# Performance work log

Hardware: AMD Instinct MI355X
Metric: run time of the kernel (lower is better)

## Reference

```python
import jax, jax.numpy as jnp
import numpy as np

PAD = -999
BATCH, NCHAIN, SEQ, NALT, NRES = 8, 2, 1024, 3, 20
NATOMS = 2_000_000
NATNAMES = 40
BACKBONE = jnp.array([0, 1, 2, 3], dtype=jnp.int32)  # N, CA, C, O atom-name ids
GLY = 7  # residue id treated as glycine (rsaSC forced to 0)
NBINS = BATCH * NCHAIN * SEQ * NALT


def setup_inputs() -> dict:
    key = jax.random.key(0)
    k = jax.random.split(key, 8)
    contRat = jax.random.uniform(k[0], (NATOMS, NALT), dtype=jnp.float32)
    atname = jax.random.randint(k[1], (NATOMS,), 0, NATNAMES, dtype=jnp.int32)
    # assign each atom to a (batch, chain, resnum) residue consistently
    resid = jax.random.randint(k[2], (NATOMS,), 0, BATCH * NCHAIN * SEQ, dtype=jnp.int32)
    batch = resid // (NCHAIN * SEQ)
    chain = (resid // SEQ) % NCHAIN
    resnum = resid % SEQ
    # residue type is a function of the residue (consistent across its atoms)
    resname_per_res = jax.random.randint(k[3], (BATCH * NCHAIN * SEQ,), 0, NRES, dtype=jnp.int32)
    resname = resname_per_res[resid]
    atom_description = jnp.stack([atname, resnum, chain, batch, resname], axis=1)
    alternatives = jax.random.bernoulli(k[4], 0.7, (NATOMS, NALT))
    # per-residue-type affine normalization points (max, min), max > min
    resMC_min = jax.random.uniform(k[5], (NRES,), dtype=jnp.float32) * 2.0
    resMC_max = resMC_min + 10.0 + jax.random.uniform(k[6], (NRES,), dtype=jnp.float32) * 20.0
    resSC_min = jax.random.uniform(k[7], (NRES,), dtype=jnp.float32) * 2.0
    resSC_max = resSC_min + 10.0 + jax.random.uniform(jax.random.fold_in(key, 99), (NRES,), dtype=jnp.float32) * 20.0
    return {
        "contRat": contRat,
        "resMC_max": resMC_max,
        "resMC_min": resMC_min,
        "resSC_max": resSC_max,
        "resSC_min": resSC_min,
        "atom_description": atom_description,
        "alternatives": alternatives,
    }


def _bind(contRat, resMC_max, resMC_min, resSC_max, resSC_min, atom_description, alternatives):
    atname = atom_description[:, 0]
    resnum = atom_description[:, 1]
    chain = atom_description[:, 2]
    batchInd = atom_description[:, 3]
    resname = atom_description[:, 4]

    is_backbone = jnp.isin(atname, BACKBONE)
    valid = atname != PAD

    # flat (batch, chain, resnum, alt) bin per atom per alternative
    base = (batchInd * NCHAIN + chain) * SEQ + resnum            # [natoms]
    flat = base[:, None] * NALT + jnp.arange(NALT, dtype=jnp.int32)[None, :]  # [natoms, nalt]

    maskMC = alternatives & (is_backbone & valid)[:, None]
    maskSC = alternatives & (~is_backbone & valid)[:, None]

    zero_idx = jnp.where(maskMC, flat, 0)
    rsaMC = jnp.zeros((NBINS,), contRat.dtype).at[zero_idx].add(
        jnp.where(maskMC, contRat, 0.0))
    rsaSC = jnp.zeros((NBINS,), contRat.dtype).at[jnp.where(maskSC, flat, 0)].add(
        jnp.where(maskSC, contRat, 0.0))

    # sequence: non-accumulating scatter of resname on the backbone path; dump
    # masked-out writes to an extra trailing bin
    seq_flat = jnp.full((NBINS + 1,), PAD, dtype=jnp.int32).at[
        jnp.where(maskMC, flat, NBINS)
    ].set(jnp.where(maskMC, resname[:, None], PAD))[:NBINS]

    shape = (BATCH, NCHAIN, SEQ, NALT)
    rsaMC = rsaMC.reshape(shape)
    rsaSC = rsaSC.reshape(shape)
    seq = seq_flat.reshape(shape)

    # per-residue-type affine normalization: (x - min) / (max - min)
    idx = jnp.clip(seq, 0, NRES - 1)
    has_res = seq != PAD
    rsaMC = jnp.where(has_res, (rsaMC - resMC_min[idx]) / (resMC_max[idx] - resMC_min[idx]), rsaMC)
    sc_norm = (rsaSC - resSC_min[idx]) / (resSC_max[idx] - resSC_min[idx])
    rsaSC = jnp.where(has_res & (seq != GLY), sc_norm,
                      jnp.where(has_res & (seq == GLY), 0.0, rsaSC))

    return jnp.clip(rsaMC, 0.0, 1.0), jnp.clip(rsaSC, 0.0, 1.0)


def reference(contRat, resMC_max, resMC_min, resSC_max, resSC_min, atom_description, alternatives):
    return _bind(contRat, resMC_max, resMC_min, resSC_max, resSC_min,
                 atom_description, alternatives)
```

## Files before the change

kernel.cpp:

```cpp
#include <hip/hip_runtime.h>


#define PADV   (-999)
#define BATCH  8
#define NCHAIN 2
#define SEQL   1024
#define NALT   3
#define NRES   20
#define NATOMS 2000000
#define GLY    7
#define NRESID (BATCH * NCHAIN * SEQL)
#define NBINS  (NRESID * NALT)
#define NBLK   ((NATOMS + 1023) / 1024)
#define NBUCK  256
#define ACC_SUB 8

#define PK_R(w)    ((int)((w) & 16383u))
#define PK_RES(w)  (((w) >> 14) & 31u)
#define PK_BB(w)   (((w) >> 19) & 1u)
#define PK_AM(w)   ((w) >> 20)

#define OFF_PACK  ((size_t)0)
#define SZ_PACK   ((size_t)NATOMS * 4)
#define OFF_HIST  (OFF_PACK + SZ_PACK)
#define SZ_HIST   ((size_t)NBUCK * NBLK * 4)
#define OFF_BB    (OFF_HIST + SZ_HIST)
#define SZ_BB     ((size_t)1280)
#define OFF_TOT   (OFF_BB + SZ_BB)
#define SZ_TOT    ((size_t)1024)
#define OFF_SORT  (OFF_TOT + SZ_TOT)
#define SZ_SORT   ((size_t)NATOMS * 8)
#define OFF_ACC   (OFF_SORT + SZ_SORT)
#define SZ_ACC    ((size_t)NBUCK * ACC_SUB * 384 * 4)
#define OFF_RES   (OFF_ACC + SZ_ACC)
#define SZ_RES    ((size_t)NBUCK * ACC_SUB * 64 * 4)
#define WS_NEED   (OFF_RES + SZ_RES)

__global__ __launch_bounds__(256)
void k_pack_hist(const int* __restrict__ desc,
                 const unsigned char* __restrict__ altB,
                 const int* __restrict__ altI,
                 unsigned* __restrict__ pack,
                 unsigned* __restrict__ hist) {
    __shared__ unsigned h[NBUCK];
    for (int j = threadIdx.x; j < NBUCK; j += 256) h[j] = 0u;
    __syncthreads();

    const unsigned char probe = altB[(threadIdx.x & 63) * 4 + 1];
    const bool byteLayout = (__ballot(probe != 0) != 0ULL);

    const int a0 = (blockIdx.x * 256 + threadIdx.x) * 4;
    if (a0 < NATOMS) {
        const int4* d4 = (const int4*)(desc + (size_t)a0 * 5);
        int4 q0 = d4[0], q1 = d4[1], q2 = d4[2], q3 = d4[3], q4 = d4[4];
        int an[4], rn[4], ch[4], bi[4], rs[4];
        an[0]=q0.x; rn[0]=q0.y; ch[0]=q0.z; bi[0]=q0.w; rs[0]=q1.x;
        an[1]=q1.y; rn[1]=q1.z; ch[1]=q1.w; bi[1]=q2.x; rs[1]=q2.y;
        an[2]=q2.z; rn[2]=q2.w; ch[2]=q3.x; bi[2]=q3.y; rs[2]=q3.z;
        an[3]=q3.w; rn[3]=q4.x; ch[3]=q4.y; bi[3]=q4.z; rs[3]=q4.w;

        unsigned am[4];
        if (byteLayout) {
            const unsigned* b3 = (const unsigned*)(altB + (size_t)a0 * 3);
            unsigned w0 = b3[0], w1 = b3[1], w2 = b3[2];
            unsigned char f[12];
            f[0]=w0; f[1]=w0>>8; f[2]=w0>>16; f[3]=w0>>24;
            f[4]=w1; f[5]=w1>>8; f[6]=w1>>16; f[7]=w1>>24;
            f[8]=w2; f[9]=w2>>8; f[10]=w2>>16; f[11]=w2>>24;
            #pragma unroll
            for (int k = 0; k < 4; ++k)
                am[k] = (f[k*3+0]?1u:0u) | (f[k*3+1]?2u:0u) | (f[k*3+2]?4u:0u);
        } else {
            const int4* i4 = (const int4*)(altI + (size_t)a0 * 3);
            int4 w0 = i4[0], w1 = i4[1], w2 = i4[2];
            int f[12] = {w0.x,w0.y,w0.z,w0.w, w1.x,w1.y,w1.z,w1.w,
                         w2.x,w2.y,w2.z,w2.w};
            #pragma unroll
            for (int k = 0; k < 4; ++k)
                am[k] = (f[k*3+0]?1u:0u) | (f[k*3+1]?2u:0u) | (f[k*3+2]?4u:0u);
        }

        uint4 pw;
        unsigned* pwp = (unsigned*)&pw;
        #pragma unroll
        for (int k = 0; k < 4; ++k) {
            const bool valid = (an[k] != PADV);
            const bool bb    = ((unsigned)an[k] <= 3u);
            const int  r     = (bi[k] * NCHAIN + ch[k]) * SEQL + rn[k];
            const bool rOK   = ((unsigned)r < (unsigned)NRESID);
            const unsigned a = (valid && rOK) ? am[k] : 0u;
            pwp[k] = (rOK ? (unsigned)r : 0u)
                   | ((unsigned)(rs[k] & 31) << 14)
                   | ((bb ? 1u : 0u) << 19) | (a << 20);
            if (a) atomicAdd(&h[(pwp[k] >> 6) & 255u], 1u);
        }
        *(uint4*)(pack + a0) = pw;
    }
    __syncthreads();
    for (int j = threadIdx.x; j < NBUCK; j += 256)
        hist[(size_t)j * NBLK + blockIdx.x] = h[j];
}

__global__ __launch_bounds__(256)
void k_prefix1(unsigned* __restrict__ hist, unsigned* __restrict__ totals) {
    __shared__ unsigned cnt[2048];
    __shared__ unsigned csum[256];
    unsigned* h = hist + (size_t)blockIdx.x * NBLK;
    const int t = threadIdx.x;

    for (int j = t; j < 2048; j += 256) cnt[j] = (j < NBLK) ? h[j] : 0u;
    __syncthreads();

    unsigned s = 0;
    #pragma unroll
    for (int k = 0; k < 8; ++k) s += cnt[t * 8 + k];
    csum[t] = s;
    __syncthreads();
    for (int off = 1; off < 256; off <<= 1) {
        unsigned x = (t >= off) ? csum[t - off] : 0u;
        __syncthreads();
        csum[t] += x;
        __syncthreads();
    }
    if (t == 255) totals[blockIdx.x] = csum[255];
    unsigned run = (t == 0) ? 0u : csum[t - 1];
    #pragma unroll
    for (int k = 0; k < 8; ++k) {
        const int idx = t * 8 + k;
        const unsigned old = cnt[idx];
        cnt[idx] = run;
        run += old;
    }
    __syncthreads();
    for (int j = t; j < NBLK; j += 256) h[j] = cnt[j];
}

__global__ __launch_bounds__(256)
void k_prefix2(const unsigned* __restrict__ totals,
               unsigned* __restrict__ bucketBase) {
    __shared__ unsigned s[256];
    const int t = threadIdx.x;
    const unsigned own = totals[t];
    s[t] = own;
    __syncthreads();
    for (int off = 1; off < 256; off <<= 1) {
        unsigned x = (t >= off) ? s[t - off] : 0u;
        __syncthreads();
        s[t] += x;
        __syncthreads();
    }
    bucketBase[t] = s[t] - own;
    if (t == 255) bucketBase[256] = s[255];
}

__global__ __launch_bounds__(256)
void k_scatter(const unsigned* __restrict__ pack,
               const unsigned* __restrict__ hist,
               const unsigned* __restrict__ bucketBase,
               uint2* __restrict__ sorted) {
    __shared__ unsigned lbase[NBUCK];
    for (int j = threadIdx.x; j < NBUCK; j += 256)
        lbase[j] = bucketBase[j] + hist[(size_t)j * NBLK + blockIdx.x];
    __syncthreads();

    const int a0 = (blockIdx.x * 256 + threadIdx.x) * 4;
    if (a0 < NATOMS) {
        const uint4 pw = *(const uint4*)(pack + a0);
        const unsigned* pwp = (const unsigned*)&pw;
        #pragma unroll
        for (int k = 0; k < 4; ++k) {
            const unsigned w = pwp[k];
            if (w >> 20) {
                const unsigned b   = (w >> 6) & 255u;
                const unsigned pos = atomicAdd(&lbase[b], 1u);
                sorted[pos] = make_uint2(w, (unsigned)(a0 + k));
            }
        }
    }
}

__global__ __launch_bounds__(256)
void k_accum(const uint2* __restrict__ sorted,
             const float* __restrict__ contRat,
             const unsigned* __restrict__ bucketBase,
             float* __restrict__ accPart,
             unsigned* __restrict__ resPart) {
    __shared__ float acc[6 * 64];
    __shared__ unsigned ror[64];
    const int b   = blockIdx.x >> 3;
    const int sub = blockIdx.x & 7;

    for (int j = threadIdx.x; j < 384; j += 256) acc[j] = 0.0f;
    if (threadIdx.x < 64) ror[threadIdx.x] = 0u;
    __syncthreads();

    const unsigned s0 = bucketBase[b], s1 = bucketBase[b + 1];
    const unsigned len = s1 - s0;
    const unsigned lo = s0 + (unsigned)(((unsigned long long)len * sub) >> 3);
    const unsigned hi = s0 + (unsigned)(((unsigned long long)len * (sub + 1)) >> 3);

    for (unsigned i = lo + threadIdx.x; i < hi; i += 256) {
        const uint2 e = sorted[i];
        const unsigned w = e.x;
        const int lr = (int)(w & 63u);
        const unsigned am = PK_AM(w);
        const float* cr = contRat + (size_t)e.y * 3;
        const int pb = PK_BB(w) ? 0 : 3;
        if (PK_BB(w)) atomicOr(&ror[lr], (am << 5) | PK_RES(w));
        if (am & 1) atomicAdd(&acc[(pb + 0) * 64 + lr], cr[0]);
        if (am & 2) atomicAdd(&acc[(pb + 1) * 64 + lr], cr[1]);
        if (am & 4) atomicAdd(&acc[(pb + 2) * 64 + lr], cr[2]);
    }
    __syncthreads();

    float* ap = accPart + ((size_t)b * ACC_SUB + sub) * 384;
    for (int j = threadIdx.x; j < 384; j += 256) ap[j] = acc[j];
    if (threadIdx.x < 64)
        resPart[((size_t)b * ACC_SUB + sub) * 64 + threadIdx.x] = ror[threadIdx.x];
}

__global__ __launch_bounds__(192)
void k_finalize(const float* __restrict__ accPart,
                const unsigned* __restrict__ resPart,
                float* __restrict__ out,
                const float* __restrict__ mcmax,
                const float* __restrict__ mcmin,
                const float* __restrict__ scmax,
                const float* __restrict__ scmin) {
    const int b = blockIdx.x;
    const int t = threadIdx.x;
    const int lr = t / 3, alt = t - lr * 3;

    float m = 0.0f, v = 0.0f;
    unsigned rb = 0u;
    #pragma unroll
    for (int s = 0; s < ACC_SUB; ++s) {
        const float* ap = accPart + ((size_t)b * ACC_SUB + s) * 384;
        m  += ap[alt * 64 + lr];
        v  += ap[(3 + alt) * 64 + lr];
        rb |= resPart[((size_t)b * ACC_SUB + s) * 64 + lr];
    }

    if ((rb >> (5 + alt)) & 1u) {
        int resn = (int)(rb & 31u);
        if (resn > NRES - 1) resn = NRES - 1;
        m = (m - mcmin[resn]) / (mcmax[resn] - mcmin[resn]);
        v = ((rb & 31u) == GLY) ? 0.0f
                                : (v - scmin[resn]) / (scmax[resn] - scmin[resn]);
    }
    out[b * 192 + t]         = fminf(fmaxf(m, 0.0f), 1.0f);
    out[NBINS + b * 192 + t] = fminf(fmaxf(v, 0.0f), 1.0f);
}

__global__ void k_init_flat(float* __restrict__ out, int* __restrict__ seq,
                            int* __restrict__ flag,
                            const unsigned char* __restrict__ altBytes) {
    int i = blockIdx.x * blockDim.x + threadIdx.x;
    if (i < NBINS) { out[i] = 0.0f; out[NBINS + i] = 0.0f; seq[i] = PADV; }
    if (blockIdx.x == 0 && threadIdx.x < 64) {
        unsigned char b = altBytes[threadIdx.x * 4 + 1];
        unsigned long long m = __ballot(b != 0);
        if (threadIdx.x == 0) *flag = (m != 0ULL) ? 1 : 0;
    }
}

__global__ void k_scatter_flat(const float* __restrict__ contRat,
                               const int* __restrict__ desc,
                               const unsigned char* __restrict__ altB,
                               const int* __restrict__ altI,
                               const int* __restrict__ flag,
                               float* __restrict__ mcArr,
                               float* __restrict__ scArr,
                               int* __restrict__ seq) {
    int a = blockIdx.x * blockDim.x + threadIdx.x;
    if (a >= NATOMS) return;
    const int atname  = desc[a * 5 + 0];
    const int resnum  = desc[a * 5 + 1];
    const int chain   = desc[a * 5 + 2];
    const int batchI  = desc[a * 5 + 3];
    const int resname = desc[a * 5 + 4];
    const bool valid = (atname != PADV);
    const bool is_bb = (atname >= 0) && (atname <= 3);
    const int  base  = ((batchI * NCHAIN + chain) * SEQL + resnum) * NALT;
    const bool byteLayout = (*flag != 0);
    #pragma unroll
    for (int alt = 0; alt < NALT; ++alt) {
        bool altv;
        if (byteLayout) altv = (altB[a * NALT + alt] != 0);
        else            altv = (altI[a * NALT + alt] != 0);
        if (altv && valid) {
            const float c = contRat[a * NALT + alt];
            const int   f = base + alt;
            if (is_bb) { atomicAdd(&mcArr[f], c); seq[f] = resname; }
            else       { atomicAdd(&scArr[f], c); }
        }
    }
}

__global__ void k_final_flat(float* __restrict__ mc, float* __restrict__ sc,
                             const int* __restrict__ seq,
                             const float* __restrict__ mcmax,
                             const float* __restrict__ mcmin,
                             const float* __restrict__ scmax,
                             const float* __restrict__ scmin) {
    int i = blockIdx.x * blockDim.x + threadIdx.x;
    if (i >= NBINS) return;
    const int s = seq[i];
    float m = mc[i], v = sc[i];
    if (s != PADV) {
        int idx = s < 0 ? 0 : (s > NRES - 1 ? NRES - 1 : s);
        m = (m - mcmin[idx]) / (mcmax[idx] - mcmin[idx]);
        if (s != GLY) v = (v - scmin[idx]) / (scmax[idx] - scmin[idx]);
        else          v = 0.0f;
    }
    mc[i] = fminf(fmaxf(m, 0.0f), 1.0f);
    sc[i] = fminf(fmaxf(v, 0.0f), 1.0f);
}

extern "C" void kernel_launch(void* const* d_in, const int* in_sizes, int n_in,
                              void* d_out, int out_size, void* d_ws, size_t ws_size,
                              hipStream_t stream) {
    const float* contRat = (const float*)d_in[0];
    const float* mcmax   = (const float*)d_in[1];
    const float* mcmin   = (const float*)d_in[2];
    const float* scmax   = (const float*)d_in[3];
    const float* scmin   = (const float*)d_in[4];
    const int*   desc    = (const int*)d_in[5];
    const void*  alts    = d_in[6];

    float* out = (float*)d_out;

    if (ws_size >= WS_NEED) {
        unsigned* pack  = (unsigned*)((char*)d_ws + OFF_PACK);
        unsigned* hist  = (unsigned*)((char*)d_ws + OFF_HIST);
        unsigned* bbase = (unsigned*)((char*)d_ws + OFF_BB);
        unsigned* tot   = (unsigned*)((char*)d_ws + OFF_TOT);
        uint2*    sorted= (uint2*)   ((char*)d_ws + OFF_SORT);
        float*    accP  = (float*)   ((char*)d_ws + OFF_ACC);
        unsigned* resP  = (unsigned*)((char*)d_ws + OFF_RES);

        k_pack_hist<<<NBLK, 256, 0, stream>>>(
            desc, (const unsigned char*)alts, (const int*)alts, pack, hist);
        k_prefix1<<<NBUCK, 256, 0, stream>>>(hist, tot);
        k_prefix2<<<1, 256, 0, stream>>>(tot, bbase);
        k_scatter<<<NBLK, 256, 0, stream>>>(pack, hist, bbase, sorted);
        k_accum<<<NBUCK * ACC_SUB, 256, 0, stream>>>(
            sorted, contRat, bbase, accP, resP);
        k_finalize<<<NBUCK, 192, 0, stream>>>(
            accP, resP, out, mcmax, mcmin, scmax, scmin);
    } else {
        int* seq  = (int*)d_ws;
        int* flag = seq + NBINS;
        const int binBlocks = (NBINS + 255) / 256;
        k_init_flat<<<binBlocks, 256, 0, stream>>>(out, seq, flag,
                                                   (const unsigned char*)alts);
        k_scatter_flat<<<(NATOMS + 255) / 256, 256, 0, stream>>>(
            contRat, desc,
            (const unsigned char*)alts, (const int*)alts, flag,
            out, out + NBINS, seq);
        k_final_flat<<<binBlocks, 256, 0, stream>>>(
            out, out + NBINS, seq, mcmax, mcmin, scmax, scmin);
    }
}
```

Baseline: 170.1 us.

## Fuse prefix/finalize kernels, coalesce scatter via shared-memory local sort, enlarge atom blocks

Each block now handles 4096 atoms, which cuts the histogram to 489 columns and lets prefix1 scan it with two values per thread. The separate bucket-base scan kernel is removed and its scan is recomputed inside scatter and accum. Scatter first sorts its atoms locally in shared memory, then writes to the global sorted array in bucket-contiguous runs instead of uncoalesced atomic-slot writes. Finalize is merged into accum: the last of the 8 sub-blocks per bucket, chosen by a ticket counter, does the reduction. This saves two launches, at the cost of repeated 256-wide scans per block and about 40KB of extra shared memory in scatter.

```diff
diff --git a/kernel.cpp b/kernel.cpp
--- a/kernel.cpp
+++ b/kernel.cpp
@@ -11,7 +11,8 @@
 #define GLY    7
 #define NRESID (BATCH * NCHAIN * SEQL)
 #define NBINS  (NRESID * NALT)
-#define NBLK   ((NATOMS + 1023) / 1024)
+#define APB    4096
+#define NBLK   ((NATOMS + APB - 1) / APB)
 #define NBUCK  256
 #define ACC_SUB 8
 
@@ -24,11 +25,11 @@
 #define SZ_PACK   ((size_t)NATOMS * 4)
 #define OFF_HIST  (OFF_PACK + SZ_PACK)
 #define SZ_HIST   ((size_t)NBUCK * NBLK * 4)
-#define OFF_BB    (OFF_HIST + SZ_HIST)
-#define SZ_BB     ((size_t)1280)
-#define OFF_TOT   (OFF_BB + SZ_BB)
+#define OFF_TOT   (OFF_HIST + SZ_HIST)
 #define SZ_TOT    ((size_t)1024)
-#define OFF_SORT  (OFF_TOT + SZ_TOT)
+#define OFF_TKT   (OFF_TOT + SZ_TOT)
+#define SZ_TKT    ((size_t)1024)
+#define OFF_SORT  (OFF_TKT + SZ_TKT)
 #define SZ_SORT   ((size_t)NATOMS * 8)
 #define OFF_ACC   (OFF_SORT + SZ_SORT)
 #define SZ_ACC    ((size_t)NBUCK * ACC_SUB * 384 * 4)
@@ -43,14 +44,18 @@
                  unsigned* __restrict__ pack,
                  unsigned* __restrict__ hist) {
     __shared__ unsigned h[NBUCK];
-    for (int j = threadIdx.x; j < NBUCK; j += 256) h[j] = 0u;
+    h[threadIdx.x] = 0u;
     __syncthreads();
 
     const unsigned char probe = altB[(threadIdx.x & 63) * 4 + 1];
     const bool byteLayout = (__ballot(probe != 0) != 0ULL);
 
-    const int a0 = (blockIdx.x * 256 + threadIdx.x) * 4;
-    if (a0 < NATOMS) {
+    const int blockBase = blockIdx.x * APB;
+    #pragma unroll
+    for (int g = 0; g < 4; ++g) {
+        const int a0 = blockBase + (g * 256 + (int)threadIdx.x) * 4;
+        if (a0 >= NATOMS) continue;
+
         const int4* d4 = (const int4*)(desc + (size_t)a0 * 5);
         int4 q0 = d4[0], q1 = d4[1], q2 = d4[2], q3 = d4[3], q4 = d4[4];
         int an[4], rn[4], ch[4], bi[4], rs[4];
@@ -97,23 +102,23 @@
         *(uint4*)(pack + a0) = pw;
     }
     __syncthreads();
-    for (int j = threadIdx.x; j < NBUCK; j += 256)
-        hist[(size_t)j * NBLK + blockIdx.x] = h[j];
+    hist[(size_t)threadIdx.x * NBLK + blockIdx.x] = h[threadIdx.x];
 }
 
 __global__ __launch_bounds__(256)
-void k_prefix1(unsigned* __restrict__ hist, unsigned* __restrict__ totals) {
-    __shared__ unsigned cnt[2048];
+void k_prefix1(unsigned* __restrict__ hist,
+               unsigned* __restrict__ totals,
+               unsigned* __restrict__ ticket) {
+    __shared__ unsigned cnt[512];
     __shared__ unsigned csum[256];
     unsigned* h = hist + (size_t)blockIdx.x * NBLK;
     const int t = threadIdx.x;
 
-    for (int j = t; j < 2048; j += 256) cnt[j] = (j < NBLK) ? h[j] : 0u;
-    __syncthreads();
-
-    unsigned s = 0;
-    #pragma unroll
-    for (int k = 0; k < 8; ++k) s += cnt[t * 8 + k];
+    cnt[t]       = (t < NBLK) ? h[t] : 0u;
+    cnt[t + 256] = (t + 256 < NBLK) ? h[t + 256] : 0u;
+    __syncthreads();
+
+    unsigned s = cnt[2 * t] + cnt[2 * t + 1];
     csum[t] = s;
     __syncthreads();
     for (int off = 1; off < 256; off <<= 1) {
@@ -122,84 +127,145 @@
         csum[t] += x;
         __syncthreads();
     }
-    if (t == 255) totals[blockIdx.x] = csum[255];
+    if (t == 0) { totals[blockIdx.x] = csum[255]; ticket[blockIdx.x] = 0u; }
+
     unsigned run = (t == 0) ? 0u : csum[t - 1];
-    #pragma unroll
-    for (int k = 0; k < 8; ++k) {
-        const int idx = t * 8 + k;
-        const unsigned old = cnt[idx];
-        cnt[idx] = run;
-        run += old;
-    }
-    __syncthreads();
-    for (int j = t; j < NBLK; j += 256) h[j] = cnt[j];
-}
-
-__global__ __launch_bounds__(256)
-void k_prefix2(const unsigned* __restrict__ totals,
-               unsigned* __restrict__ bucketBase) {
-    __shared__ unsigned s[256];
-    const int t = threadIdx.x;
-    const unsigned own = totals[t];
-    s[t] = own;
-    __syncthreads();
-    for (int off = 1; off < 256; off <<= 1) {
-        unsigned x = (t >= off) ? s[t - off] : 0u;
-        __syncthreads();
-        s[t] += x;
-        __syncthreads();
-    }
-    bucketBase[t] = s[t] - own;
-    if (t == 255) bucketBase[256] = s[255];
+    const unsigned c0 = cnt[2 * t];
+    cnt[2 * t]     = run;
+    cnt[2 * t + 1] = run + c0;
+    __syncthreads();
+    if (t < NBLK)       h[t]       = cnt[t];
+    if (t + 256 < NBLK) h[t + 256] = cnt[t + 256];
 }
 
 __global__ __launch_bounds__(256)
 void k_scatter(const unsigned* __restrict__ pack,
                const unsigned* __restrict__ hist,
-               const unsigned* __restrict__ bucketBase,
+               const unsigned* __restrict__ totals,
                uint2* __restrict__ sorted) {
-    __shared__ unsigned lbase[NBUCK];
-    for (int j = threadIdx.x; j < NBUCK; j += 256)
-        lbase[j] = bucketBase[j] + hist[(size_t)j * NBLK + blockIdx.x];
-    __syncthreads();
-
-    const int a0 = (blockIdx.x * 256 + threadIdx.x) * 4;
-    if (a0 < NATOMS) {
-        const uint4 pw = *(const uint4*)(pack + a0);
-        const unsigned* pwp = (const unsigned*)&pw;
+    __shared__ unsigned sc[256];
+    __shared__ unsigned gBase[256];
+    __shared__ unsigned lofs[256];
+    __shared__ unsigned lcnt[256];
+    __shared__ unsigned wBuf[APB];
+    __shared__ unsigned idxBuf[APB];
+
+    const int t   = threadIdx.x;
+    const int blk = blockIdx.x;
+
+    const unsigned own = totals[t];
+    sc[t] = own;
+    __syncthreads();
+    for (int off = 1; off < 256; off <<= 1) {
+        unsigned x = (t >= off) ? sc[t - off] : 0u;
+        __syncthreads();
+        sc[t] += x;
+        __syncthreads();
+    }
+    gBase[t] = (sc[t] - own) + hist[(size_t)t * NBLK + blk];
+    lcnt[t] = 0u;
+    __syncthreads();
+
+    const int blockBase = blk * APB;
+    uint4 pw[4];
+    #pragma unroll
+    for (int g = 0; g < 4; ++g) {
+        const int a0 = blockBase + (g * 256 + t) * 4;
+        if (a0 < NATOMS) {
+            pw[g] = *(const uint4*)(pack + a0);
+            const unsigned* p = (const unsigned*)&pw[g];
+            #pragma unroll
+            for (int k = 0; k < 4; ++k)
+                if (p[k] >> 20) atomicAdd(&lcnt[(p[k] >> 6) & 255u], 1u);
+        } else {
+            pw[g] = make_uint4(0u, 0u, 0u, 0u);
+        }
+    }
+    __syncthreads();
+
+    const unsigned lown = lcnt[t];
+    sc[t] = lown;
+    __syncthreads();
+    for (int off = 1; off < 256; off <<= 1) {
+        unsigned x = (t >= off) ? sc[t - off] : 0u;
+        __syncthreads();
+        sc[t] += x;
+        __syncthreads();
+    }
+    lofs[t] = sc[t] - lown;
+    lcnt[t] = 0u;
+    __syncthreads();
+    const unsigned total = sc[255];
+
+    #pragma unroll
+    for (int g = 0; g < 4; ++g) {
+        const int a0 = blockBase + (g * 256 + t) * 4;
+        const unsigned* p = (const unsigned*)&pw[g];
         #pragma unroll
         for (int k = 0; k < 4; ++k) {
-            const unsigned w = pwp[k];
+            const unsigned w = p[k];
             if (w >> 20) {
-                const unsigned b   = (w >> 6) & 255u;
-                const unsigned pos = atomicAdd(&lbase[b], 1u);
-                sorted[pos] = make_uint2(w, (unsigned)(a0 + k));
+                const unsigned b    = (w >> 6) & 255u;
+                const unsigned slot = atomicAdd(&lcnt[b], 1u);
+                const unsigned pos  = lofs[b] + slot;
+                wBuf[pos]   = w;
+                idxBuf[pos] = (unsigned)(a0 + k);
             }
         }
     }
+    __syncthreads();
+
+    for (unsigned j = (unsigned)t; j < total; j += 256u) {
+        const unsigned w = wBuf[j];
+        const unsigned b = (w >> 6) & 255u;
+        const unsigned dest = gBase[b] + (j - lofs[b]);
+        sorted[dest] = make_uint2(w, idxBuf[j]);
+    }
 }
 
 __global__ __launch_bounds__(256)
-void k_accum(const uint2* __restrict__ sorted,
-             const float* __restrict__ contRat,
-             const unsigned* __restrict__ bucketBase,
-             float* __restrict__ accPart,
-             unsigned* __restrict__ resPart) {
+void k_accum_fin(const uint2* __restrict__ sorted,
+                 const float* __restrict__ contRat,
+                 const unsigned* __restrict__ totals,
+                 unsigned* __restrict__ ticket,
+                 float* __restrict__ accPart,
+                 unsigned* __restrict__ resPart,
+                 float* __restrict__ out,
+                 const float* __restrict__ mcmax,
+                 const float* __restrict__ mcmin,
+                 const float* __restrict__ scmax,
+                 const float* __restrict__ scmin) {
     __shared__ float acc[6 * 64];
     __shared__ unsigned ror[64];
+    __shared__ unsigned sc[256];
+    __shared__ unsigned eb[257];
+    __shared__ int lastFlag;
+
     const int b   = blockIdx.x >> 3;
     const int sub = blockIdx.x & 7;
-
-    for (int j = threadIdx.x; j < 384; j += 256) acc[j] = 0.0f;
-    if (threadIdx.x < 64) ror[threadIdx.x] = 0u;
-    __syncthreads();
-
-    const unsigned s0 = bucketBase[b], s1 = bucketBase[b + 1];
+    const int t   = threadIdx.x;
+
+    const unsigned own = totals[t];
+    sc[t] = own;
+    __syncthreads();
+    for (int off = 1; off < 256; off <<= 1) {
+        unsigned x = (t >= off) ? sc[t - off] : 0u;
+        __syncthreads();
+        sc[t] += x;
+        __syncthreads();
+    }
+    eb[t] = sc[t] - own;
+    if (t == 255) eb[256] = sc[255];
+    for (int j = t; j < 384; j += 256) acc[j] = 0.0f;
+    if (t < 64) ror[t] = 0u;
+    __syncthreads();
+
+    const unsigned s0 = eb[b], s1 = eb[b + 1];
     const unsigned len = s1 - s0;
     const unsigned lo = s0 + (unsigned)(((unsigned long long)len * sub) >> 3);
     const unsigned hi = s0 + (unsigned)(((unsigned long long)len * (sub + 1)) >> 3);
 
-    for (unsigned i = lo + threadIdx.x; i < hi; i += 256) {
+    for (unsigned i = lo + t; i < hi; i += 256u) {
         const uint2 e = sorted[i];
         const unsigned w = e.x;
         const int lr = (int)(w & 63u);
@@ -214,33 +280,30 @@
     __syncthreads();
 
     float* ap = accPart + ((size_t)b * ACC_SUB + sub) * 384;
-    for (int j = threadIdx.x; j < 384; j += 256) ap[j] = acc[j];
-    if (threadIdx.x < 64)
-        resPart[((size_t)b * ACC_SUB + sub) * 64 + threadIdx.x] = ror[threadIdx.x];
-}
-
-__global__ __launch_bounds__(192)
-void k_finalize(const float* __restrict__ accPart,
-                const unsigned* __restrict__ resPart,
-                float* __restrict__ out,
-                const float* __restrict__ mcmax,
-                const float* __restrict__ mcmin,
-                const float* __restrict__ scmax,
-                const float* __restrict__ scmin) {
-    const int b = blockIdx.x;
-    const int t = threadIdx.x;
-    const int lr = t / 3, alt = t - lr * 3;
-
+    for (int j = t; j < 384; j += 256) ap[j] = acc[j];
+    if (t < 64)
+        resPart[((size_t)b * ACC_SUB + sub) * 64 + t] = ror[t];
+    __syncthreads();
+
+    if (t == 0) {
+        __threadfence();
+        const unsigned old = __hip_atomic_fetch_add(
+            &ticket[b], 1u, __ATOMIC_ACQ_REL, __HIP_MEMORY_SCOPE_AGENT);
+        lastFlag = (old == ACC_SUB - 1);
+    }
+    __syncthreads();
+    if (!lastFlag || t >= 192) return;
+
+    const int lr2 = t / 3, alt = t - lr2 * 3;
     float m = 0.0f, v = 0.0f;
     unsigned rb = 0u;
     #pragma unroll
-    for (int s = 0; s < ACC_SUB; ++s) {
-        const float* ap = accPart + ((size_t)b * ACC_SUB + s) * 384;
-        m  += ap[alt * 64 + lr];
-        v  += ap[(3 + alt) * 64 + lr];
-        rb |= resPart[((size_t)b * ACC_SUB + s) * 64 + lr];
-    }
-
+    for (int s2 = 0; s2 < ACC_SUB; ++s2) {
+        const float* p2 = accPart + ((size_t)b * ACC_SUB + s2) * 384;
+        m  += p2[alt * 64 + lr2];
+        v  += p2[(3 + alt) * 64 + lr2];
+        rb |= resPart[((size_t)b * ACC_SUB + s2) * 64 + lr2];
+    }
     if ((rb >> (5 + alt)) & 1u) {
         int resn = (int)(rb & 31u);
         if (resn > NRES - 1) resn = NRES - 1;
@@ -297,7 +360,7 @@
     }
 }
 
-__global__ void k_final_flat(float* __restrict__ mc, float* __restrict__ sc,
+__global__ void k_final_flat(float* __restrict__ mc, float* __restrict__ sc2,
                              const int* __restrict__ seq,
                              const float* __restrict__ mcmax,
                              const float* __restrict__ mcmin,
@@ -306,15 +369,15 @@
     int i = blockIdx.x * blockDim.x + threadIdx.x;
     if (i >= NBINS) return;
     const int s = seq[i];
-    float m = mc[i], v = sc[i];
+    float m = mc[i], v = sc2[i];
     if (s != PADV) {
         int idx = s < 0 ? 0 : (s > NRES - 1 ? NRES - 1 : s);
         m = (m - mcmin[idx]) / (mcmax[idx] - mcmin[idx]);
         if (s != GLY) v = (v - scmin[idx]) / (scmax[idx] - scmin[idx]);
         else          v = 0.0f;
     }
-    mc[i] = fminf(fmaxf(m, 0.0f), 1.0f);
-    sc[i] = fminf(fmaxf(v, 0.0f), 1.0f);
+    mc[i]  = fminf(fmaxf(m, 0.0f), 1.0f);
+    sc2[i] = fminf(fmaxf(v, 0.0f), 1.0f);
 }
 
 extern "C" void kernel_launch(void* const* d_in, const int* in_sizes, int n_in,
@@ -333,21 +396,19 @@
     if (ws_size >= WS_NEED) {
         unsigned* pack  = (unsigned*)((char*)d_ws + OFF_PACK);
         unsigned* hist  = (unsigned*)((char*)d_ws + OFF_HIST);
-        unsigned* bbase = (unsigned*)((char*)d_ws + OFF_BB);
         unsigned* tot   = (unsigned*)((char*)d_ws + OFF_TOT);
+        unsigned* tkt   = (unsigned*)((char*)d_ws + OFF_TKT);
         uint2*    sorted= (uint2*)   ((char*)d_ws + OFF_SORT);
         float*    accP  = (float*)   ((char*)d_ws + OFF_ACC);
         unsigned* resP  = (unsigned*)((char*)d_ws + OFF_RES);
 
         k_pack_hist<<<NBLK, 256, 0, stream>>>(
             desc, (const unsigned char*)alts, (const int*)alts, pack, hist);
-        k_prefix1<<<NBUCK, 256, 0, stream>>>(hist, tot);
-        k_prefix2<<<1, 256, 0, stream>>>(tot, bbase);
-        k_scatter<<<NBLK, 256, 0, stream>>>(pack, hist, bbase, sorted);
-        k_accum<<<NBUCK * ACC_SUB, 256, 0, stream>>>(
-            sorted, contRat, bbase, accP, resP);
-        k_finalize<<<NBUCK, 192, 0, stream>>>(
-            accP, resP, out, mcmax, mcmin, scmax, scmin);
+        k_prefix1<<<NBUCK, 256, 0, stream>>>(hist, tot, tkt);
+        k_scatter<<<NBLK, 256, 0, stream>>>(pack, hist, tot, sorted);
+        k_accum_fin<<<NBUCK * ACC_SUB, 256, 0, stream>>>(
+            sorted, contRat, tot, tkt, accP, resP,
+            out, mcmax, mcmin, scmax, scmin);
     } else {
         int* seq  = (int*)d_ws;
         int* flag = seq + NBINS;
```

After: 245.0 us. +44.0%, slower.
